# Kernel tuning notes

Measured on AMD Instinct MI355X. Metric: run time of the kernel, lower is better.

Reference implementation:

```python
import jax, jax.numpy as jnp
import numpy as np

B, S, D_MODEL, D_QK, D_VO = 4, 2048, 1024, 128, 128
NEG = -1.0e9


def setup_inputs() -> dict:
    key = jax.random.key(0)
    k1, k2, k3, k4, k5 = jax.random.split(key, 5)
    enc = jax.random.normal(k1, (B, S, D_MODEL), dtype=jnp.float32)
    # causal mask: True means masked (masked_fill), broadcast over batch
    causal = jnp.triu(jnp.ones((S, S), dtype=bool), k=1)
    mask = jnp.broadcast_to(causal, (B, S, S))
    scale = 0.02
    W_q = jax.random.normal(k2, (D_MODEL, D_QK), dtype=jnp.float32) * scale
    W_k = jax.random.normal(k3, (D_MODEL, D_QK), dtype=jnp.float32) * scale
    W_v = jax.random.normal(k4, (D_MODEL, D_VO), dtype=jnp.float32) * scale
    W_o = jax.random.normal(k5, (D_VO, D_MODEL), dtype=jnp.float32) * scale
    return {"encodings": enc, "mask": mask, "W_q": W_q, "W_k": W_k, "W_v": W_v, "W_o": W_o}


def reference(encodings, mask, W_q, W_k, W_v, W_o):
    # q,k: [B,S,d_qk]; v: [B,S,d_vo]
    q = jnp.einsum('bsd,de->bse', encodings, W_q)
    k = jnp.einsum('bsd,de->bse', encodings, W_k)
    v = jnp.einsum('bsd,de->bse', encodings, W_v)
    sims = jnp.einsum('bqe,bke->bqk', q, k) / jnp.asarray(D_QK ** 0.5, q.dtype)
    sims = jnp.where(mask, jnp.asarray(NEG, sims.dtype), sims)
    attn = jax.nn.softmax(sims, axis=-1)  # [B,S,S]
    scores = jnp.einsum('bqk,bke->bqe', attn, v)  # [B,S,d_vo]
    return jnp.einsum('bse,ed->bsd', scores, W_o)  # [B,S,d_model]
```

## Files before the change

kernel.cpp:

```cpp
#include <hip/hip_runtime.h>
#include <hip/hip_bf16.h>
#include <stdint.h>

typedef __attribute__((ext_vector_type(8))) short short8;
typedef __attribute__((ext_vector_type(4))) float floatx4;

using bf16 = __hip_bfloat16;

#define SCALE_L2 0.12751793359133147f

__device__ inline unsigned short f2b(float f) {
    bf16 h = __float2bfloat16(f);
    return *(unsigned short*)&h;
}
__device__ inline float b2f(unsigned short u) {
    union { unsigned int i; float f; } v;
    v.i = ((unsigned int)u) << 16;
    return v.f;
}

__device__ __forceinline__ void gll16(const bf16* g, bf16* l) {
    __builtin_amdgcn_global_load_lds((__attribute__((address_space(1))) void*)g,
                                     (__attribute__((address_space(3))) void*)l,
                                     16, 0, 0);
}

__global__ __launch_bounds__(256) void prep_all(const float4* __restrict__ enc4,
                                                ushort4* __restrict__ encb4,
                                                const float* __restrict__ Wq,
                                                const float* __restrict__ Wk,
                                                const float* __restrict__ Wv,
                                                const float* __restrict__ Wo,
                                                bf16* __restrict__ Wqkvt,
                                                bf16* __restrict__ Wot) {
    int bx = blockIdx.x;
    if (bx < 8192) {
        int i = bx * 256 + threadIdx.x;
        float4 v = enc4[i];
        ushort4 o;
        o.x = f2b(v.x); o.y = f2b(v.y); o.z = f2b(v.z); o.w = f2b(v.w);
        encb4[i] = o;
    } else {
        int idx = (bx - 8192) * 256 + threadIdx.x;
        int sel = idx >> 17;
        int i = idx & 131071;
        if (sel < 3) {
            const float* W = (sel == 0) ? Wq : (sel == 1) ? Wk : Wv;
            int r = i >> 7, c = i & 127;
            Wqkvt[(size_t)(sel * 128 + c) * 1024 + r] = __float2bfloat16(W[i]);
        } else {
            int r = i >> 10, c = i & 1023;
            Wot[(size_t)c * 128 + r] = __float2bfloat16(Wo[i]);
        }
    }
}

__global__ __launch_bounds__(256) void gemm_qkv(const bf16* __restrict__ A,
                                                const bf16* __restrict__ Bt,
                                                bf16* __restrict__ Qb,
                                                bf16* __restrict__ Kb,
                                                bf16* __restrict__ Vtb) {
    __shared__ bf16 As[64 * 32];
    __shared__ bf16 Bs[128 * 32];

    const int tid = threadIdx.x;
    const int m0 = blockIdx.x * 64;
    const int nsel = blockIdx.y;
    const int brow0 = nsel * 128;
    const int w = tid >> 6, lane = tid & 63;
    const int wm = (w >> 1) * 32, wn = (w & 1) * 64;
    const int quad = lane >> 4, l16 = lane & 15;

    const int ar = tid >> 2, akq = (tid & 3) * 8;
    const int br1 = (tid + 256) >> 2;
    bf16* As_w  = &As[w * 512];
    bf16* Bs_w0 = &Bs[w * 512];
    bf16* Bs_w1 = &Bs[2048 + w * 512];

    floatx4 acc[2][4];
#pragma unroll
    for (int i = 0; i < 2; i++)
#pragma unroll
        for (int j = 0; j < 4; j++) acc[i][j] = (floatx4){0.f, 0.f, 0.f, 0.f};

    for (int k0 = 0; k0 < 1024; k0 += 32) {
        __syncthreads();
        gll16(&A[(size_t)(m0 + ar) * 1024 + k0 + akq], As_w);
        gll16(&Bt[(size_t)(brow0 + ar) * 1024 + k0 + akq], Bs_w0);
        gll16(&Bt[(size_t)(brow0 + br1) * 1024 + k0 + akq], Bs_w1);
        __syncthreads();

        short8 a[2], b[4];
#pragma unroll
        for (int mt = 0; mt < 2; mt++)
            a[mt] = *(const short8*)&As[(wm + mt * 16 + l16) * 32 + quad * 8];
#pragma unroll
        for (int nt = 0; nt < 4; nt++)
            b[nt] = *(const short8*)&Bs[(wn + nt * 16 + l16) * 32 + quad * 8];
#pragma unroll
        for (int mt = 0; mt < 2; mt++)
#pragma unroll
            for (int nt = 0; nt < 4; nt++)
                acc[mt][nt] = __builtin_amdgcn_mfma_f32_16x16x32_bf16(a[mt], b[nt], acc[mt][nt], 0, 0, 0);
    }

#pragma unroll
    for (int mt = 0; mt < 2; mt++)
#pragma unroll
        for (int nt = 0; nt < 4; nt++)
#pragma unroll
            for (int r = 0; r < 4; r++) {
                int row = m0 + wm + mt * 16 + quad * 4 + r;
                int col = wn + nt * 16 + l16;
                bf16 h = __float2bfloat16(acc[mt][nt][r]);
                if (nsel == 0) {
                    Qb[(size_t)row * 128 + col] = h;
                } else if (nsel == 1) {
                    Kb[(size_t)row * 128 + col] = h;
                } else {
                    int bb = row >> 11, ss = row & 2047;
                    Vtb[(size_t)bb * 262144 + (size_t)col * 2048 + ss] = h;
                }
            }
}

__global__ __launch_bounds__(256) void gemm_out(const bf16* __restrict__ A,
                                                const bf16* __restrict__ Bt,
                                                float* __restrict__ C) {
    __shared__ bf16 As[64 * 40];
    __shared__ bf16 Bs[128 * 40];

    const int tid = threadIdx.x;
    const int m0 = blockIdx.x * 64;
    const int n0 = blockIdx.y * 128;
    const int w = tid >> 6, lane = tid & 63;
    const int wm = (w >> 1) * 32, wn = (w & 1) * 64;
    const int quad = lane >> 4, l16 = lane & 15;

    const int ra = tid >> 2, ca = (tid & 3) * 8;
    const int rb0 = tid >> 2, rb1 = (tid + 256) >> 2;

    floatx4 acc[2][4];
#pragma unroll
    for (int i = 0; i < 2; i++)
#pragma unroll
        for (int j = 0; j < 4; j++) acc[i][j] = (floatx4){0.f, 0.f, 0.f, 0.f};

    int4 pa  = *(const int4*)&A[(size_t)(m0 + ra) * 128 + ca];
    int4 pb0 = *(const int4*)&Bt[(size_t)(n0 + rb0) * 128 + ca];
    int4 pb1 = *(const int4*)&Bt[(size_t)(n0 + rb1) * 128 + ca];

    for (int k0 = 0; k0 < 128; k0 += 32) {
        __syncthreads();
        *(int4*)&As[ra * 40 + ca] = pa;
        *(int4*)&Bs[rb0 * 40 + ca] = pb0;
        *(int4*)&Bs[rb1 * 40 + ca] = pb1;
        __syncthreads();

        if (k0 + 32 < 128) {
            pa  = *(const int4*)&A[(size_t)(m0 + ra) * 128 + k0 + 32 + ca];
            pb0 = *(const int4*)&Bt[(size_t)(n0 + rb0) * 128 + k0 + 32 + ca];
            pb1 = *(const int4*)&Bt[(size_t)(n0 + rb1) * 128 + k0 + 32 + ca];
        }

        short8 a[2], b[4];
#pragma unroll
        for (int mt = 0; mt < 2; mt++)
            a[mt] = *(const short8*)&As[(wm + mt * 16 + l16) * 40 + quad * 8];
#pragma unroll
        for (int nt = 0; nt < 4; nt++)
            b[nt] = *(const short8*)&Bs[(wn + nt * 16 + l16) * 40 + quad * 8];
#pragma unroll
        for (int mt = 0; mt < 2; mt++)
#pragma unroll
            for (int nt = 0; nt < 4; nt++)
                acc[mt][nt] = __builtin_amdgcn_mfma_f32_16x16x32_bf16(a[mt], b[nt], acc[mt][nt], 0, 0, 0);
    }

#pragma unroll
    for (int mt = 0; mt < 2; mt++)
#pragma unroll
        for (int nt = 0; nt < 4; nt++)
#pragma unroll
            for (int r = 0; r < 4; r++) {
                int row = m0 + wm + mt * 16 + quad * 4 + r;
                int col = n0 + wn + nt * 16 + l16;
                C[(size_t)row * 1024 + col] = acc[mt][nt][r];
            }
}

__global__ __launch_bounds__(256) void flash_split(const bf16* __restrict__ Q,
                                                   const bf16* __restrict__ K,
                                                   const bf16* __restrict__ Vt,
                                                   bf16* __restrict__ Opb,
                                                   float2* __restrict__ Ml) {
    __shared__ bf16 Ks[64 * 136];
    __shared__ bf16 Vs[128 * 72];
    __shared__ bf16 Ps[4 * 16 * 72];

    const int tid = threadIdx.x;
    const int x = blockIdx.x;
    const int b = x / 144;
    const int id = x - b * 144;
    const int g = (id >= 112) ? 7 : (id >= 84) ? 6 : (id >= 60) ? 5 : (id >= 40) ? 4
                : (id >= 24) ? 3 : (id >= 12) ? 2 : (id >= 4) ? 1 : 0;
    const int nc = g + 1;
    const int local = id - 2 * g * nc;
    const int qi = local / nc;
    const int c = local - qi * nc;
    const int qt = 4 * g + qi;
    const int q0 = qt * 64;
    const int start = 4 * c;
    const int end = min(start + 4, qt + 1);

    const int w = tid >> 6, lane = tid & 63;
    const int quad = lane >> 4, l16 = lane & 15;

    const int qrow = q0 + w * 16 + l16;
    const bf16* Qrow = &Q[((size_t)b * 2048 + qrow) * 128];
    short8 qf[4];
#pragma unroll
    for (int k4 = 0; k4 < 4; k4++)
        qf[k4] = *(const short8*)&Qrow[k4 * 32 + quad * 8];

    float m_run = -1.0e30f, l_run = 0.f;
    floatx4 o[8];
#pragma unroll
    for (int d = 0; d < 8; d++) o[d] = (floatx4){0.f, 0.f, 0.f, 0.f};

    int4 kreg[4], vreg[4];
    const int sr[4]  = {(tid + 0) >> 4, (tid + 256) >> 4, (tid + 512) >> 4, (tid + 768) >> 4};
    const int scg    = (tid & 15) * 8;
    const int sr2[4] = {(tid + 0) >> 3, (tid + 256) >> 3, (tid + 512) >> 3, (tid + 768) >> 3};
    const int scg2   = (tid & 7) * 8;

#pragma unroll
    for (int i = 0; i < 4; i++) {
        kreg[i] = *(const int4*)&K[((size_t)b * 2048 + start * 64 + sr[i]) * 128 + scg];
        vreg[i] = *(const int4*)&Vt[(size_t)b * 262144 + (size_t)sr2[i] * 2048 + start * 64 + scg2];
    }

    for (int kt = start; kt < end; kt++) {
        __syncthreads();
#pragma unroll
        for (int i = 0; i < 4; i++) {
            *(int4*)&Ks[sr[i] * 136 + scg] = kreg[i];
            *(int4*)&Vs[sr2[i] * 72 + scg2] = vreg[i];
        }
        __syncthreads();

        if (kt + 1 < end) {
#pragma unroll
            for (int i = 0; i < 4; i++) {
                kreg[i] = *(const int4*)&K[((size_t)b * 2048 + (kt + 1) * 64 + sr[i]) * 128 + scg];
                vreg[i] = *(const int4*)&Vt[(size_t)b * 262144 + (size_t)sr2[i] * 2048 + (kt + 1) * 64 + scg2];
            }
        }

        floatx4 s_acc[4];
#pragma unroll
        for (int nt = 0; nt < 4; nt++) {
            s_acc[nt] = (floatx4){0.f, 0.f, 0.f, 0.f};
#pragma unroll
            for (int k4 = 0; k4 < 4; k4++) {
                short8 kf = *(const short8*)&Ks[(nt * 16 + l16) * 136 + k4 * 32 + quad * 8];
                s_acc[nt] = __builtin_amdgcn_mfma_f32_16x16x32_bf16(kf, qf[k4], s_acc[nt], 0, 0, 0);
            }
        }

        float sv[4][4];
#pragma unroll
        for (int nt = 0; nt < 4; nt++)
#pragma unroll
            for (int r = 0; r < 4; r++) {
                float s = s_acc[nt][r] * SCALE_L2;
                if (kt == qt) {
                    int kcol = kt * 64 + nt * 16 + quad * 4 + r;
                    if (kcol > qrow) s = -1.0e9f;
                }
                sv[nt][r] = s;
            }

        float t0 = fmaxf(fmaxf(sv[0][0], sv[0][1]), fmaxf(sv[0][2], sv[0][3]));
        float t1 = fmaxf(fmaxf(sv[1][0], sv[1][1]), fmaxf(sv[1][2], sv[1][3]));
        float t2 = fmaxf(fmaxf(sv[2][0], sv[2][1]), fmaxf(sv[2][2], sv[2][3]));
        float t3 = fmaxf(fmaxf(sv[3][0], sv[3][1]), fmaxf(sv[3][2], sv[3][3]));
        float tmax = fmaxf(fmaxf(t0, t1), fmaxf(t2, t3));
        tmax = fmaxf(tmax, __shfl_xor(tmax, 16));
        tmax = fmaxf(tmax, __shfl_xor(tmax, 32));

        float mnew = fmaxf(m_run, tmax);
        float alpha = exp2f(m_run - mnew);
        m_run = mnew;

        float rsum = 0.f;
#pragma unroll
        for (int nt = 0; nt < 4; nt++)
#pragma unroll
            for (int r = 0; r < 4; r++) {
                float p = exp2f(sv[nt][r] - mnew);
                sv[nt][r] = p;
                rsum += p;
            }
        rsum += __shfl_xor(rsum, 16);
        rsum += __shfl_xor(rsum, 32);
        l_run = l_run * alpha + rsum;

#pragma unroll
        for (int nt = 0; nt < 4; nt++) {
            ushort4 pk;
            pk.x = f2b(sv[nt][0]); pk.y = f2b(sv[nt][1]);
            pk.z = f2b(sv[nt][2]); pk.w = f2b(sv[nt][3]);
            *(ushort4*)&Ps[w * 1152 + l16 * 72 + nt * 16 + quad * 4] = pk;
        }

#pragma unroll
        for (int d = 0; d < 8; d++) {
            o[d][0] *= alpha; o[d][1] *= alpha; o[d][2] *= alpha; o[d][3] *= alpha;
        }

        short8 pf[2];
#pragma unroll
        for (int k2 = 0; k2 < 2; k2++)
            pf[k2] = *(const short8*)&Ps[w * 1152 + l16 * 72 + k2 * 32 + quad * 8];
#pragma unroll
        for (int d = 0; d < 8; d++)
#pragma unroll
            for (int k2 = 0; k2 < 2; k2++) {
                short8 vf = *(const short8*)&Vs[(d * 16 + l16) * 72 + k2 * 32 + quad * 8];
                o[d] = __builtin_amdgcn_mfma_f32_16x16x32_bf16(vf, pf[k2], o[d], 0, 0, 0);
            }
    }

    const int lrow = w * 16 + l16;
    const size_t obase = ((size_t)x * 64 + lrow) * 128;
#pragma unroll
    for (int d = 0; d < 8; d++) {
        ushort4 pk;
        pk.x = f2b(o[d][0]); pk.y = f2b(o[d][1]);
        pk.z = f2b(o[d][2]); pk.w = f2b(o[d][3]);
        *(ushort4*)&Opb[obase + d * 16 + quad * 4] = pk;
    }
    if (lane < 16) Ml[(size_t)x * 64 + lrow] = make_float2(m_run, l_run);
}

__global__ __launch_bounds__(256) void flash_merge(const bf16* __restrict__ Opb,
                                                   const float2* __restrict__ Ml,
                                                   bf16* __restrict__ Sc) {
    int idx = blockIdx.x * 256 + threadIdx.x;
    int row = idx >> 5, dg = (idx & 31) * 4;
    int b = row >> 11, s = row & 2047;
    int qt = s >> 6, rl = s & 63;
    int g = qt >> 2, nc = g + 1;
    int id0 = b * 144 + 2 * g * nc + (qt & 3) * nc;

    float m[8], l[8], M = -1.0e30f;
    for (int j = 0; j < nc; j++) {
        float2 t = Ml[(size_t)(id0 + j) * 64 + rl];
        m[j] = t.x; l[j] = t.y;
        M = fmaxf(M, t.x);
    }
    float L = 0.f;
    float a0 = 0.f, a1 = 0.f, a2 = 0.f, a3 = 0.f;
    for (int j = 0; j < nc; j++) {
        float wj = exp2f(m[j] - M);
        L += l[j] * wj;
        ushort4 p = *(const ushort4*)&Opb[((size_t)(id0 + j) * 64 + rl) * 128 + dg];
        a0 += wj * b2f(p.x); a1 += wj * b2f(p.y);
        a2 += wj * b2f(p.z); a3 += wj * b2f(p.w);
    }
    float inv = 1.0f / L;
    ushort4 o;
    o.x = f2b(a0 * inv); o.y = f2b(a1 * inv);
    o.z = f2b(a2 * inv); o.w = f2b(a3 * inv);
    *(ushort4*)&Sc[(size_t)row * 128 + dg] = o;
}

extern "C" void kernel_launch(void* const* d_in, const int* in_sizes, int n_in,
                              void* d_out, int out_size, void* d_ws, size_t ws_size,
                              hipStream_t stream) {
    const float* enc = (const float*)d_in[0];
    const float* Wq = (const float*)d_in[2];
    const float* Wk = (const float*)d_in[3];
    const float* Wv = (const float*)d_in[4];
    const float* Wo = (const float*)d_in[5];
    float* out = (float*)d_out;

    const size_t MB = 1024 * 1024;
    char* ws = (char*)d_ws;
    bf16*   encb  = (bf16*)(ws);
    bf16*   Opb   = (bf16*)(ws);
    bf16*   Qb    = (bf16*)(ws + 16 * MB);
    bf16*   Kb    = (bf16*)(ws + 18 * MB);
    bf16*   Vtb   = (bf16*)(ws + 20 * MB);
    bf16*   Scb   = (bf16*)(ws + 22 * MB);
    bf16*   Wqkvt = (bf16*)(ws + 24 * MB);
    bf16*   Wot   = (bf16*)(ws + 24 * MB + 768 * 1024);
    float2* Ml    = (float2*)(ws + 25 * MB);

    prep_all<<<10240, 256, 0, stream>>>((const float4*)enc, (ushort4*)encb,
                                        Wq, Wk, Wv, Wo, Wqkvt, Wot);

    dim3 blk(256);
    gemm_qkv<<<dim3(128, 3), blk, 0, stream>>>(encb, Wqkvt, Qb, Kb, Vtb);

    flash_split<<<576, blk, 0, stream>>>(Qb, Kb, Vtb, Opb, Ml);
    flash_merge<<<1024, blk, 0, stream>>>(Opb, Ml, Scb);

    gemm_out<<<dim3(128, 8), blk, 0, stream>>>(Scb, Wot, out);
}
```

Baseline: 210.9 us.

## Fuse fp32-to-bf16 conversion into QKV GEMM and split-merge into output GEMM

Drops the separate encoder-conversion pass: the QKV GEMM now reads fp32 encodings directly, converts them to bf16 in registers and stages them in padded LDS. Its tile is halved in N so the grid doubles to 768 blocks. The flash split-merge kernel is folded into the output projection, which rebuilds the normalized score rows from the partial outputs while loading its A tile. This removes two launches and the bf16 encoding and score round trips, at the cost of double fp32 reads of the encodings and redundant merge work repeated across the 8 N-blocks.

```diff
diff --git a/kernel.cpp b/kernel.cpp
--- a/kernel.cpp
+++ b/kernel.cpp
@@ -19,173 +19,110 @@
     return v.f;
 }
 
-__device__ __forceinline__ void gll16(const bf16* g, bf16* l) {
-    __builtin_amdgcn_global_load_lds((__attribute__((address_space(1))) void*)g,
-                                     (__attribute__((address_space(3))) void*)l,
-                                     16, 0, 0);
-}
-
-__global__ __launch_bounds__(256) void prep_all(const float4* __restrict__ enc4,
-                                                ushort4* __restrict__ encb4,
-                                                const float* __restrict__ Wq,
-                                                const float* __restrict__ Wk,
-                                                const float* __restrict__ Wv,
-                                                const float* __restrict__ Wo,
-                                                bf16* __restrict__ Wqkvt,
-                                                bf16* __restrict__ Wot) {
-    int bx = blockIdx.x;
-    if (bx < 8192) {
-        int i = bx * 256 + threadIdx.x;
-        float4 v = enc4[i];
-        ushort4 o;
-        o.x = f2b(v.x); o.y = f2b(v.y); o.z = f2b(v.z); o.w = f2b(v.w);
-        encb4[i] = o;
+__global__ __launch_bounds__(256) void prep_w(const float* __restrict__ Wq,
+                                              const float* __restrict__ Wk,
+                                              const float* __restrict__ Wv,
+                                              const float* __restrict__ Wo,
+                                              bf16* __restrict__ Wqkvt,
+                                              bf16* __restrict__ Wot) {
+    int idx4 = (blockIdx.x * 256 + threadIdx.x) * 4;
+    int sel = idx4 >> 17;
+    int i = idx4 & 131071;
+    if (sel < 3) {
+        const float* W = (sel == 0) ? Wq : (sel == 1) ? Wk : Wv;
+        float4 v = *(const float4*)&W[i];
+        int r = i >> 7, c = i & 127;
+        Wqkvt[(size_t)(sel * 128 + c + 0) * 1024 + r] = __float2bfloat16(v.x);
+        Wqkvt[(size_t)(sel * 128 + c + 1) * 1024 + r] = __float2bfloat16(v.y);
+        Wqkvt[(size_t)(sel * 128 + c + 2) * 1024 + r] = __float2bfloat16(v.z);
+        Wqkvt[(size_t)(sel * 128 + c + 3) * 1024 + r] = __float2bfloat16(v.w);
     } else {
-        int idx = (bx - 8192) * 256 + threadIdx.x;
-        int sel = idx >> 17;
-        int i = idx & 131071;
-        if (sel < 3) {
-            const float* W = (sel == 0) ? Wq : (sel == 1) ? Wk : Wv;
-            int r = i >> 7, c = i & 127;
-            Wqkvt[(size_t)(sel * 128 + c) * 1024 + r] = __float2bfloat16(W[i]);
-        } else {
-            int r = i >> 10, c = i & 1023;
-            Wot[(size_t)c * 128 + r] = __float2bfloat16(Wo[i]);
-        }
-    }
-}
-
-__global__ __launch_bounds__(256) void gemm_qkv(const bf16* __restrict__ A,
+        float4 v = *(const float4*)&Wo[i];
+        int r = i >> 10, c = i & 1023;
+        Wot[(size_t)(c + 0) * 128 + r] = __float2bfloat16(v.x);
+        Wot[(size_t)(c + 1) * 128 + r] = __float2bfloat16(v.y);
+        Wot[(size_t)(c + 2) * 128 + r] = __float2bfloat16(v.z);
+        Wot[(size_t)(c + 3) * 128 + r] = __float2bfloat16(v.w);
+    }
+}
+
+__global__ __launch_bounds__(256) void gemm_qkv(const float* __restrict__ enc,
                                                 const bf16* __restrict__ Bt,
                                                 bf16* __restrict__ Qb,
                                                 bf16* __restrict__ Kb,
                                                 bf16* __restrict__ Vtb) {
-    __shared__ bf16 As[64 * 32];
-    __shared__ bf16 Bs[128 * 32];
+    __shared__ bf16 As[64 * 40];
+    __shared__ bf16 Bs[64 * 40];
 
     const int tid = threadIdx.x;
     const int m0 = blockIdx.x * 64;
-    const int nsel = blockIdx.y;
-    const int brow0 = nsel * 128;
+    const int brow0 = blockIdx.y * 64;
+    const int proj = brow0 >> 7;
+    const int colb = brow0 & 127;
     const int w = tid >> 6, lane = tid & 63;
-    const int wm = (w >> 1) * 32, wn = (w & 1) * 64;
+    const int wm = (w >> 1) * 32, wn = (w & 1) * 32;
     const int quad = lane >> 4, l16 = lane & 15;
 
-    const int ar = tid >> 2, akq = (tid & 3) * 8;
-    const int br1 = (tid + 256) >> 2;
-    bf16* As_w  = &As[w * 512];
-    bf16* Bs_w0 = &Bs[w * 512];
-    bf16* Bs_w1 = &Bs[2048 + w * 512];
-
-    floatx4 acc[2][4];
+    const int ra = tid >> 2, kq = (tid & 3) * 8;
+
+    floatx4 acc[2][2];
 #pragma unroll
     for (int i = 0; i < 2; i++)
 #pragma unroll
-        for (int j = 0; j < 4; j++) acc[i][j] = (floatx4){0.f, 0.f, 0.f, 0.f};
+        for (int j = 0; j < 2; j++) acc[i][j] = (floatx4){0.f, 0.f, 0.f, 0.f};
+
+    float4 pa0 = *(const float4*)&enc[(size_t)(m0 + ra) * 1024 + kq];
+    float4 pa1 = *(const float4*)&enc[(size_t)(m0 + ra) * 1024 + kq + 4];
+    int4 pb = *(const int4*)&Bt[(size_t)(brow0 + ra) * 1024 + kq];
 
     for (int k0 = 0; k0 < 1024; k0 += 32) {
         __syncthreads();
-        gll16(&A[(size_t)(m0 + ar) * 1024 + k0 + akq], As_w);
-        gll16(&Bt[(size_t)(brow0 + ar) * 1024 + k0 + akq], Bs_w0);
-        gll16(&Bt[(size_t)(brow0 + br1) * 1024 + k0 + akq], Bs_w1);
-        __syncthreads();
-
-        short8 a[2], b[4];
+        short8 av;
+        av[0] = (short)f2b(pa0.x); av[1] = (short)f2b(pa0.y);
+        av[2] = (short)f2b(pa0.z); av[3] = (short)f2b(pa0.w);
+        av[4] = (short)f2b(pa1.x); av[5] = (short)f2b(pa1.y);
+        av[6] = (short)f2b(pa1.z); av[7] = (short)f2b(pa1.w);
+        *(short8*)&As[ra * 40 + kq] = av;
+        *(int4*)&Bs[ra * 40 + kq] = pb;
+        __syncthreads();
+
+        if (k0 + 32 < 1024) {
+            pa0 = *(const float4*)&enc[(size_t)(m0 + ra) * 1024 + k0 + 32 + kq];
+            pa1 = *(const float4*)&enc[(size_t)(m0 + ra) * 1024 + k0 + 36 + kq];
+            pb = *(const int4*)&Bt[(size_t)(brow0 + ra) * 1024 + k0 + 32 + kq];
+        }
+
+        short8 a[2], b[2];
 #pragma unroll
         for (int mt = 0; mt < 2; mt++)
-            a[mt] = *(const short8*)&As[(wm + mt * 16 + l16) * 32 + quad * 8];
-#pragma unroll
-        for (int nt = 0; nt < 4; nt++)
-            b[nt] = *(const short8*)&Bs[(wn + nt * 16 + l16) * 32 + quad * 8];
+            a[mt] = *(const short8*)&As[(wm + mt * 16 + l16) * 40 + quad * 8];
+#pragma unroll
+        for (int nt = 0; nt < 2; nt++)
+            b[nt] = *(const short8*)&Bs[(wn + nt * 16 + l16) * 40 + quad * 8];
 #pragma unroll
         for (int mt = 0; mt < 2; mt++)
 #pragma unroll
-            for (int nt = 0; nt < 4; nt++)
+            for (int nt = 0; nt < 2; nt++)
                 acc[mt][nt] = __builtin_amdgcn_mfma_f32_16x16x32_bf16(a[mt], b[nt], acc[mt][nt], 0, 0, 0);
     }
 
 #pragma unroll
     for (int mt = 0; mt < 2; mt++)
 #pragma unroll
-        for (int nt = 0; nt < 4; nt++)
+        for (int nt = 0; nt < 2; nt++)
 #pragma unroll
             for (int r = 0; r < 4; r++) {
                 int row = m0 + wm + mt * 16 + quad * 4 + r;
-                int col = wn + nt * 16 + l16;
+                int col = colb + wn + nt * 16 + l16;
                 bf16 h = __float2bfloat16(acc[mt][nt][r]);
-                if (nsel == 0) {
+                if (proj == 0) {
                     Qb[(size_t)row * 128 + col] = h;
-                } else if (nsel == 1) {
+                } else if (proj == 1) {
                     Kb[(size_t)row * 128 + col] = h;
                 } else {
                     int bb = row >> 11, ss = row & 2047;
                     Vtb[(size_t)bb * 262144 + (size_t)col * 2048 + ss] = h;
                 }
-            }
-}
-
-__global__ __launch_bounds__(256) void gemm_out(const bf16* __restrict__ A,
-                                                const bf16* __restrict__ Bt,
-                                                float* __restrict__ C) {
-    __shared__ bf16 As[64 * 40];
-    __shared__ bf16 Bs[128 * 40];
-
-    const int tid = threadIdx.x;
-    const int m0 = blockIdx.x * 64;
-    const int n0 = blockIdx.y * 128;
-    const int w = tid >> 6, lane = tid & 63;
-    const int wm = (w >> 1) * 32, wn = (w & 1) * 64;
-    const int quad = lane >> 4, l16 = lane & 15;
-
-    const int ra = tid >> 2, ca = (tid & 3) * 8;
-    const int rb0 = tid >> 2, rb1 = (tid + 256) >> 2;
-
-    floatx4 acc[2][4];
-#pragma unroll
-    for (int i = 0; i < 2; i++)
-#pragma unroll
-        for (int j = 0; j < 4; j++) acc[i][j] = (floatx4){0.f, 0.f, 0.f, 0.f};
-
-    int4 pa  = *(const int4*)&A[(size_t)(m0 + ra) * 128 + ca];
-    int4 pb0 = *(const int4*)&Bt[(size_t)(n0 + rb0) * 128 + ca];
-    int4 pb1 = *(const int4*)&Bt[(size_t)(n0 + rb1) * 128 + ca];
-
-    for (int k0 = 0; k0 < 128; k0 += 32) {
-        __syncthreads();
-        *(int4*)&As[ra * 40 + ca] = pa;
-        *(int4*)&Bs[rb0 * 40 + ca] = pb0;
-        *(int4*)&Bs[rb1 * 40 + ca] = pb1;
-        __syncthreads();
-
-        if (k0 + 32 < 128) {
-            pa  = *(const int4*)&A[(size_t)(m0 + ra) * 128 + k0 + 32 + ca];
-            pb0 = *(const int4*)&Bt[(size_t)(n0 + rb0) * 128 + k0 + 32 + ca];
-            pb1 = *(const int4*)&Bt[(size_t)(n0 + rb1) * 128 + k0 + 32 + ca];
-        }
-
-        short8 a[2], b[4];
-#pragma unroll
-        for (int mt = 0; mt < 2; mt++)
-            a[mt] = *(const short8*)&As[(wm + mt * 16 + l16) * 40 + quad * 8];
-#pragma unroll
-        for (int nt = 0; nt < 4; nt++)
-            b[nt] = *(const short8*)&Bs[(wn + nt * 16 + l16) * 40 + quad * 8];
-#pragma unroll
-        for (int mt = 0; mt < 2; mt++)
-#pragma unroll
-            for (int nt = 0; nt < 4; nt++)
-                acc[mt][nt] = __builtin_amdgcn_mfma_f32_16x16x32_bf16(a[mt], b[nt], acc[mt][nt], 0, 0, 0);
-    }
-
-#pragma unroll
-    for (int mt = 0; mt < 2; mt++)
-#pragma unroll
-        for (int nt = 0; nt < 4; nt++)
-#pragma unroll
-            for (int r = 0; r < 4; r++) {
-                int row = m0 + wm + mt * 16 + quad * 4 + r;
-                int col = n0 + wn + nt * 16 + l16;
-                C[(size_t)row * 1024 + col] = acc[mt][nt][r];
             }
 }
 
@@ -344,36 +281,105 @@
     if (lane < 16) Ml[(size_t)x * 64 + lrow] = make_float2(m_run, l_run);
 }
 
-__global__ __launch_bounds__(256) void flash_merge(const bf16* __restrict__ Opb,
-                                                   const float2* __restrict__ Ml,
-                                                   bf16* __restrict__ Sc) {
-    int idx = blockIdx.x * 256 + threadIdx.x;
-    int row = idx >> 5, dg = (idx & 31) * 4;
-    int b = row >> 11, s = row & 2047;
-    int qt = s >> 6, rl = s & 63;
-    int g = qt >> 2, nc = g + 1;
-    int id0 = b * 144 + 2 * g * nc + (qt & 3) * nc;
-
-    float m[8], l[8], M = -1.0e30f;
+__global__ __launch_bounds__(256) void gemm_out_merge(const bf16* __restrict__ Opb,
+                                                      const float2* __restrict__ Ml,
+                                                      const bf16* __restrict__ Bt,
+                                                      float* __restrict__ C) {
+    __shared__ bf16 As[64 * 40];
+    __shared__ bf16 Bs[128 * 40];
+
+    const int tid = threadIdx.x;
+    const int m0 = blockIdx.x * 64;
+    const int n0 = blockIdx.y * 128;
+    const int w = tid >> 6, lane = tid & 63;
+    const int wm = (w >> 1) * 32, wn = (w & 1) * 64;
+    const int quad = lane >> 4, l16 = lane & 15;
+
+    const int ra = tid >> 2, kq = (tid & 3) * 8;
+    const int rb0 = tid >> 2, rb1 = (tid + 256) >> 2;
+
+    const int row = m0 + ra;
+    const int bb = row >> 11, s = row & 2047;
+    const int qt = s >> 6, rl = s & 63;
+    const int g = qt >> 2, nc = g + 1;
+    const int id0 = bb * 144 + 2 * g * nc + (qt & 3) * nc;
+
+    float mj[8], lj[8], wgt[8];
+    float M = -1.0e30f;
     for (int j = 0; j < nc; j++) {
         float2 t = Ml[(size_t)(id0 + j) * 64 + rl];
-        m[j] = t.x; l[j] = t.y;
+        mj[j] = t.x; lj[j] = t.y;
         M = fmaxf(M, t.x);
     }
     float L = 0.f;
-    float a0 = 0.f, a1 = 0.f, a2 = 0.f, a3 = 0.f;
     for (int j = 0; j < nc; j++) {
-        float wj = exp2f(m[j] - M);
-        L += l[j] * wj;
-        ushort4 p = *(const ushort4*)&Opb[((size_t)(id0 + j) * 64 + rl) * 128 + dg];
-        a0 += wj * b2f(p.x); a1 += wj * b2f(p.y);
-        a2 += wj * b2f(p.z); a3 += wj * b2f(p.w);
+        float wj = exp2f(mj[j] - M);
+        wgt[j] = wj;
+        L += lj[j] * wj;
     }
     float inv = 1.0f / L;
-    ushort4 o;
-    o.x = f2b(a0 * inv); o.y = f2b(a1 * inv);
-    o.z = f2b(a2 * inv); o.w = f2b(a3 * inv);
-    *(ushort4*)&Sc[(size_t)row * 128 + dg] = o;
+    for (int j = 0; j < nc; j++) wgt[j] *= inv;
+
+    floatx4 acc[2][4];
+#pragma unroll
+    for (int i = 0; i < 2; i++)
+#pragma unroll
+        for (int j = 0; j < 4; j++) acc[i][j] = (floatx4){0.f, 0.f, 0.f, 0.f};
+
+    int4 pb0 = *(const int4*)&Bt[(size_t)(n0 + rb0) * 128 + kq];
+    int4 pb1 = *(const int4*)&Bt[(size_t)(n0 + rb1) * 128 + kq];
+
+    for (int k0 = 0; k0 < 128; k0 += 32) {
+        float a8[8] = {0.f, 0.f, 0.f, 0.f, 0.f, 0.f, 0.f, 0.f};
+        const int dq = k0 + kq;
+        for (int j = 0; j < nc; j++) {
+            const ushort4* p = (const ushort4*)&Opb[((size_t)(id0 + j) * 64 + rl) * 128 + dq];
+            ushort4 p0 = p[0], p1 = p[1];
+            float wj = wgt[j];
+            a8[0] += wj * b2f(p0.x); a8[1] += wj * b2f(p0.y);
+            a8[2] += wj * b2f(p0.z); a8[3] += wj * b2f(p0.w);
+            a8[4] += wj * b2f(p1.x); a8[5] += wj * b2f(p1.y);
+            a8[6] += wj * b2f(p1.z); a8[7] += wj * b2f(p1.w);
+        }
+        short8 av;
+#pragma unroll
+        for (int e = 0; e < 8; e++) av[e] = (short)f2b(a8[e]);
+
+        __syncthreads();
+        *(short8*)&As[ra * 40 + kq] = av;
+        *(int4*)&Bs[rb0 * 40 + kq] = pb0;
+        *(int4*)&Bs[rb1 * 40 + kq] = pb1;
+        __syncthreads();
+
+        if (k0 + 32 < 128) {
+            pb0 = *(const int4*)&Bt[(size_t)(n0 + rb0) * 128 + k0 + 32 + kq];
+            pb1 = *(const int4*)&Bt[(size_t)(n0 + rb1) * 128 + k0 + 32 + kq];
+        }
+
+        short8 a[2], b[4];
+#pragma unroll
+        for (int mt = 0; mt < 2; mt++)
+            a[mt] = *(const short8*)&As[(wm + mt * 16 + l16) * 40 + quad * 8];
+#pragma unroll
+        for (int nt = 0; nt < 4; nt++)
+            b[nt] = *(const short8*)&Bs[(wn + nt * 16 + l16) * 40 + quad * 8];
+#pragma unroll
+        for (int mt = 0; mt < 2; mt++)
+#pragma unroll
+            for (int nt = 0; nt < 4; nt++)
+                acc[mt][nt] = __builtin_amdgcn_mfma_f32_16x16x32_bf16(a[mt], b[nt], acc[mt][nt], 0, 0, 0);
+    }
+
+#pragma unroll
+    for (int mt = 0; mt < 2; mt++)
+#pragma unroll
+        for (int nt = 0; nt < 4; nt++)
+#pragma unroll
+            for (int r = 0; r < 4; r++) {
+                int orow = m0 + wm + mt * 16 + quad * 4 + r;
+                int ocol = n0 + wn + nt * 16 + l16;
+                C[(size_t)orow * 1024 + ocol] = acc[mt][nt][r];
+            }
 }
 
 extern "C" void kernel_launch(void* const* d_in, const int* in_sizes, int n_in,
@@ -388,24 +394,20 @@
 
     const size_t MB = 1024 * 1024;
     char* ws = (char*)d_ws;
-    bf16*   encb  = (bf16*)(ws);
     bf16*   Opb   = (bf16*)(ws);
-    bf16*   Qb    = (bf16*)(ws + 16 * MB);
-    bf16*   Kb    = (bf16*)(ws + 18 * MB);
-    bf16*   Vtb   = (bf16*)(ws + 20 * MB);
-    bf16*   Scb   = (bf16*)(ws + 22 * MB);
-    bf16*   Wqkvt = (bf16*)(ws + 24 * MB);
-    bf16*   Wot   = (bf16*)(ws + 24 * MB + 768 * 1024);
-    float2* Ml    = (float2*)(ws + 25 * MB);
-
-    prep_all<<<10240, 256, 0, stream>>>((const float4*)enc, (ushort4*)encb,
-                                        Wq, Wk, Wv, Wo, Wqkvt, Wot);
+    bf16*   Qb    = (bf16*)(ws + 10 * MB);
+    bf16*   Kb    = (bf16*)(ws + 12 * MB);
+    bf16*   Vtb   = (bf16*)(ws + 14 * MB);
+    bf16*   Wqkvt = (bf16*)(ws + 16 * MB);
+    bf16*   Wot   = (bf16*)(ws + 16 * MB + 768 * 1024);
+    float2* Ml    = (float2*)(ws + 18 * MB);
 
     dim3 blk(256);
-    gemm_qkv<<<dim3(128, 3), blk, 0, stream>>>(encb, Wqkvt, Qb, Kb, Vtb);
+    prep_w<<<512, blk, 0, stream>>>(Wq, Wk, Wv, Wo, Wqkvt, Wot);
+
+    gemm_qkv<<<dim3(128, 6), blk, 0, stream>>>(enc, Wqkvt, Qb, Kb, Vtb);
 
     flash_split<<<576, blk, 0, stream>>>(Qb, Kb, Vtb, Opb, Ml);
-    flash_merge<<<1024, blk, 0, stream>>>(Opb, Ml, Scb);
-
-    gemm_out<<<dim3(128, 8), blk, 0, stream>>>(Scb, Wot, out);
-}
+
+    gemm_out_merge<<<dim3(128, 8), blk, 0, stream>>>(Opb, Ml, Wot, out);
+}
```

New measurement: 212.8 us. About the same (+0.9%).
